# Performance work log

Hardware: AMD Instinct MI355X
Metric: run time of the kernel (lower is better)

## Reference

```python
import jax, jax.numpy as jnp
import numpy as np

H, NH, HD = 1024, 16, 64
WIN = 256
W = WIN // 2  # one-sided window
EXP = 4
PAD_VAL = 0.0  # pad_token_id
B, S0 = 2, 2048
NEG = float(np.finfo(np.float32).min)


def setup_inputs() -> dict:
    key = jax.random.key(0)
    ks = jax.random.split(key, 12)

    def lin(k, fi, fo):
        k1, k2 = jax.random.split(k)
        w = jax.random.normal(k1, (fi, fo), jnp.float32) / np.float32(np.sqrt(fi))
        b = jax.random.normal(k2, (fo,), jnp.float32) * 0.02
        return w, b

    x = jax.random.normal(ks[0], (B, S0, H), jnp.float32)
    mask = jnp.zeros((B, S0), jnp.int32)  # 0 = real token, 1 = pad
    wq, bq = lin(ks[1], H, H)
    wk, bk = lin(ks[2], H, H)
    wv, bv = lin(ks[3], H, H)
    wqg, bqg = lin(ks[4], H, H)
    wkg, bkg = lin(ks[5], H, H)
    wvg, bvg = lin(ks[6], H, H)
    ln_g = jnp.ones((H,), jnp.float32)
    ln_b = jnp.zeros((H,), jnp.float32)
    w1, b1 = lin(ks[7], H, H * EXP)
    w2, b2 = lin(ks[8], H * EXP, H)
    return dict(x=x, mask=mask, wq=wq, bq=bq, wk=wk, bk=bk, wv=wv, bv=bv,
                wqg=wqg, bqg=bqg, wkg=wkg, bkg=bkg, wvg=wvg, bvg=bvg,
                ln_g=ln_g, ln_b=ln_b, w1=w1, b1=b1, w2=w2, b2=b2)


def _forward(x, mask, wq, bq, wk, bk, wv, bv, wqg, bqg, wkg, bkg, wvg, bvg,
             ln_g, ln_b, w1, b1, w2, b2):
    Bsz, s0, _ = x.shape
    pad = WIN - s0 % WIN
    xp = jnp.pad(x, ((0, 0), (0, pad), (0, 0)), constant_values=PAD_VAL)
    m = jnp.pad(mask, ((0, 0), (0, pad)), constant_values=1)
    S = s0 + pad
    lm = (m * -10000).at[:, -1].set(10000)  # [B,S]; task='cls': last token global
    is_masked = lm < 0
    remove = lm != 0  # masked OR global keys removed from local windows

    inv_sqrt = np.float32(1.0 / np.sqrt(HD))
    q = ((xp @ wq + bq) * inv_sqrt).reshape(Bsz, S, NH, HD)
    k = (xp @ wk + bk).reshape(Bsz, S, NH, HD)
    v = (xp @ wv + bv).reshape(Bsz, S, NH, HD)

    nc = S // W
    # chunked banded scores: query chunk of W attends to 3W keys (prev/self/next)
    qc = q.transpose(0, 2, 1, 3).reshape(Bsz, NH, nc, W, HD)
    kpad = jnp.pad(k.transpose(0, 2, 1, 3), ((0, 0), (0, 0), (W, W), (0, 0)))
    idx3w = jnp.arange(nc)[:, None] * W + jnp.arange(3 * W)[None, :]  # [nc,3W]
    kc = kpad[:, :, idx3w]  # [B,NH,nc,3W,HD]
    sc = jnp.einsum('bhcpd,bhckd->bhcpk', qc, kc)  # [B,NH,nc,W,3W]
    p_idx = jnp.arange(W)[:, None]
    d_idx = jnp.arange(2 * W + 1)[None, :]
    band = sc[:, :, :, p_idx, p_idx + d_idx]  # [B,NH,nc,W,2W+1]
    band = band.reshape(Bsz, NH, S, 2 * W + 1).transpose(0, 2, 1, 3)  # [B,S,NH,2W+1]

    # key index j = i + d - W for offset d in [0, 2W]
    j = jnp.arange(S)[:, None] + jnp.arange(2 * W + 1)[None, :] - W
    in_range = (j >= 0) & (j < S)
    jc = jnp.clip(j, 0, S - 1)
    fmask = jnp.where(remove, NEG, 0.0)  # [B,S]
    band = band + fmask[:, jc][:, :, None, :]
    band = jnp.where(in_range[None, :, None, :], band, -jnp.inf)

    # global key column (single global token = last position), concatenated in front
    gcol = jnp.einsum('bshd,bhd->bsh', q, k[:, -1])[..., None]  # [B,S,NH,1]
    scores = jnp.concatenate([gcol, band], axis=-1)  # [B,S,NH,2W+2]
    probs = jax.nn.softmax(scores, axis=-1)
    probs = jnp.where(is_masked[:, :, None, None], 0.0, probs)

    out_g = probs[..., 0][..., None] * v[:, -1][:, None]  # [B,S,NH,HD]
    lp = probs[..., 1:].transpose(0, 2, 1, 3).reshape(Bsz, NH, nc, W, 2 * W + 1)
    pc = jnp.zeros((Bsz, NH, nc, W, 3 * W), probs.dtype).at[:, :, :, p_idx, p_idx + d_idx].set(lp)
    vpad = jnp.pad(v.transpose(0, 2, 1, 3), ((0, 0), (0, 0), (W, W), (0, 0)))
    vc = vpad[:, :, idx3w]  # [B,NH,nc,3W,HD]
    out_l = jnp.einsum('bhcpk,bhckd->bhcpd', pc, vc).reshape(Bsz, NH, S, HD).transpose(0, 2, 1, 3)
    attn = (out_l + out_g).reshape(Bsz, S, H)

    # full global attention for the global token (separate projections)
    qg = ((xp[:, -1] @ wqg + bqg) * inv_sqrt).reshape(Bsz, NH, HD)
    kg = (xp @ wkg + bkg).reshape(Bsz, S, NH, HD)
    vg = (xp @ wvg + bvg).reshape(Bsz, S, NH, HD)
    gs = jnp.einsum('bhd,bshd->bhs', qg, kg)
    gs = jnp.where(is_masked[:, None, :], NEG, gs)
    gout = jnp.einsum('bhs,bshd->bhd', jax.nn.softmax(gs, axis=-1), vg).reshape(Bsz, H)
    attn = attn.at[:, -1].set(gout)

    y = (xp + attn)[:, :s0]  # residual then strip padding
    mu = y.mean(-1, keepdims=True)
    var = ((y - mu) ** 2).mean(-1, keepdims=True)
    y = (y - mu) * jax.lax.rsqrt(var + 1e-5) * ln_g + ln_b
    h = jax.nn.gelu(y @ w1 + b1, approximate=False)
    return y + (h @ w2 + b2)


def reference(x, mask, wq, bq, wk, bk, wv, bv, wqg, bqg, wkg, bkg, wvg, bvg,
              ln_g, ln_b, w1, b1, w2, b2):
    return _forward(x, mask, wq, bq, wk, bk, wv, bv, wqg, bqg, wkg, bkg,
                    wvg, bvg, ln_g, ln_b, w1, b1, w2, b2)
```

## Files before the change

kernel.cpp:

```cpp
#include <hip/hip_runtime.h>


using bf16x8 = __attribute__((ext_vector_type(8))) short;
using bf16x4 = __attribute__((ext_vector_type(4))) short;
using f32x4  = __attribute__((ext_vector_type(4))) float;

__device__ __forceinline__ float b2f(short s) {
    return __uint_as_float(((unsigned int)(unsigned short)s) << 16);
}
__device__ __forceinline__ short f2b(float f) {
    unsigned int u = __float_as_uint(f);
    u += 0x7fffu + ((u >> 16) & 1u);
    return (short)(u >> 16);
}
__device__ __forceinline__ f32x4 mfma16(bf16x8 a, bf16x8 b, f32x4 c) {
    return __builtin_amdgcn_mfma_f32_16x16x32_bf16(a, b, c, 0, 0, 0);
}
__device__ __forceinline__ float safe_exp(float x) {
    return __expf((x <= 0.f) ? x : 0.f);
}
__device__ __forceinline__ float fast_gelu(float v) {
    float z  = fabsf(v) * 0.70710678118f;
    float t  = __builtin_amdgcn_rcpf(fmaf(0.47047f, z, 1.f));
    float e  = __expf(-z * z);
    float p  = t * fmaf(t, fmaf(t, 0.7478556f, -0.0958798f), 0.3480242f);
    float er = fmaf(-p, e, 1.f);
    er = (v < 0.f) ? -er : er;
    return 0.5f * v * (1.f + er);
}
__device__ __forceinline__ void load_lds16(const short* g, short* l) {
    __builtin_amdgcn_global_load_lds((const __attribute__((address_space(1))) void*)g,
                                     (__attribute__((address_space(3))) void*)l, 16, 0, 0);
}
__device__ __forceinline__ void barrier_lds_only() {
    asm volatile("s_waitcnt lgkmcnt(0)" ::: "memory");
    __builtin_amdgcn_s_barrier();
    asm volatile("" ::: "memory");
}
#define NEGF (-3.0e38f)

__global__ void cvt_f32_bf16(const float* __restrict__ in, short* __restrict__ out, int n) {
    int i = (blockIdx.x * 256 + threadIdx.x) * 4;
    f32x4 v = *(const f32x4*)(in + i);
    bf16x4 o;
#pragma unroll
    for (int j = 0; j < 4; ++j) o[j] = f2b(v[j]);
    *(bf16x4*)(out + i) = o;
}

__global__ void cvt_transpose(const float* __restrict__ in, short* __restrict__ out,
                              int R, int C) {
    __shared__ short tile[32][33];
    int bx = blockIdx.x * 32, by = blockIdx.y * 32;
    int tx = threadIdx.x, ty = threadIdx.y;
    for (int i = ty; i < 32; i += 8)
        tile[i][tx] = f2b(in[(size_t)(by + i) * C + bx + tx]);
    __syncthreads();
    for (int i = ty; i < 32; i += 8)
        out[(size_t)(bx + i) * R + by + tx] = tile[tx][i];
}

__global__ void cvt_transpose_qkv(const float* __restrict__ wq, const float* __restrict__ wk,
                                  const float* __restrict__ wv, short* __restrict__ out) {
    __shared__ short tile[32][33];
    const float* in = (blockIdx.z == 0) ? wq : (blockIdx.z == 1) ? wk : wv;
    short* dst = out + (size_t)blockIdx.z * 1024 * 1024;
    int bx = blockIdx.x * 32, by = blockIdx.y * 32;
    int tx = threadIdx.x, ty = threadIdx.y;
    for (int i = ty; i < 32; i += 8)
        tile[i][tx] = f2b(in[(size_t)(by + i) * 1024 + bx + tx]);
    __syncthreads();
    for (int i = ty; i < 32; i += 8)
        dst[(size_t)(bx + i) * 1024 + by + tx] = tile[tx][i];
}

__global__ __launch_bounds__(256, 4) void gemm_bt(
    const short* __restrict__ A, const short* __restrict__ Bt,
    const float* __restrict__ bias0, const float* __restrict__ bias1,
    const float* __restrict__ bias2,
    short* __restrict__ C, short* __restrict__ Vt,
    int M, int N, int K, float scale, int mode)
{
    __shared__ short sh[128 * 136];
    short* As = sh;
    short* Bs = sh + 8192;
    int m0 = blockIdx.x * 128, n0 = blockIdx.y * 128;
    int t = threadIdx.x;
    int wave = t >> 6, lane = t & 63, quad = lane >> 4, l16 = lane & 15;
    int wr = (wave >> 1) * 64, wc = (wave & 1) * 64;

    const short* ap[4]; const short* bp[4]; short* la[4]; short* lb[4];
    int gk = (((lane & 7) ^ (lane >> 3)) * 8);
#pragma unroll
    for (int l = 0; l < 4; ++l) {
        int c = wave * 4 + l;
        int row = c * 8 + (lane >> 3);
        ap[l] = A  + (size_t)(m0 + row) * K + gk;
        bp[l] = Bt + (size_t)(n0 + row) * K + gk;
        la[l] = As + c * 512;
        lb[l] = Bs + c * 512;
    }
    int sw = l16 & 7;

    f32x4 acc[4][4] = {};
    for (int k0 = 0; k0 < K; k0 += 64) {
#pragma unroll
        for (int l = 0; l < 4; ++l) { load_lds16(ap[l] + k0, la[l]); load_lds16(bp[l] + k0, lb[l]); }
        __syncthreads();
#pragma unroll
        for (int ks = 0; ks < 2; ++ks) {
            int slot = ((ks * 4 + quad) ^ sw) * 8;
            bf16x8 af[4], bfr[4];
#pragma unroll
            for (int i = 0; i < 4; ++i)
                af[i] = *(bf16x8*)(As + (wr + i * 16 + l16) * 64 + slot);
#pragma unroll
            for (int j = 0; j < 4; ++j)
                bfr[j] = *(bf16x8*)(Bs + (wc + j * 16 + l16) * 64 + slot);
#pragma unroll
            for (int i = 0; i < 4; ++i)
#pragma unroll
                for (int j = 0; j < 4; ++j)
                    acc[i][j] = mfma16(af[i], bfr[j], acc[i][j]);
        }
        __syncthreads();
    }

    int seg0 = n0 >> 10;
    if (mode == 1 || seg0 < 2) {
        if (mode == 1) {
#pragma unroll
            for (int j = 0; j < 4; ++j) {
                int col = n0 + wc + j * 16 + l16;
                float bs = bias0[col];
#pragma unroll
                for (int i = 0; i < 4; ++i)
#pragma unroll
                    for (int r = 0; r < 4; ++r) {
                        float v = fast_gelu(acc[i][j][r] + bs);
                        sh[(wr + i * 16 + quad * 4 + r) * 136 + wc + j * 16 + l16] = f2b(v);
                    }
            }
        } else {
            float sc = (seg0 == 0) ? scale : 1.0f;
            const float* bpt = (seg0 == 0) ? bias0 : bias1;
#pragma unroll
            for (int j = 0; j < 4; ++j) {
                int col = n0 + wc + j * 16 + l16;
                float bs = bpt[col & 1023];
#pragma unroll
                for (int i = 0; i < 4; ++i)
#pragma unroll
                    for (int r = 0; r < 4; ++r)
                        sh[(wr + i * 16 + quad * 4 + r) * 136 + wc + j * 16 + l16] =
                            f2b((acc[i][j][r] + bs) * sc);
            }
        }
        __syncthreads();
        int row = t >> 1, half = t & 1;
        const short* src = sh + row * 136 + half * 64;
        short* dst = C + (size_t)(m0 + row) * N + n0 + half * 64;
#pragma unroll
        for (int cgk = 0; cgk < 8; ++cgk)
            *(bf16x8*)(dst + cgk * 8) = *(const bf16x8*)(src + cgk * 8);
    } else {
#pragma unroll
        for (int j = 0; j < 4; ++j) {
            int cl = wc + j * 16 + l16;
            float bs = bias2[(n0 & 1023) + cl];
#pragma unroll
            for (int i = 0; i < 4; ++i)
#pragma unroll
                for (int r = 0; r < 4; ++r)
                    sh[cl * 136 + wr + i * 16 + quad * 4 + r] = f2b(acc[i][j][r] + bs);
        }
        __syncthreads();
        int h0 = (n0 & 1023) >> 6;
        int bb = m0 >> 11, s0 = m0 & 2047;
        int sc = t & 15;
#pragma unroll
        for (int cgk = 0; cgk < 8; ++cgk) {
            int cl = (t >> 4) + cgk * 16;
            int h = h0 + (cl >> 6), d = cl & 63;
            *(bf16x8*)(Vt + (((size_t)(bb * 16 + h)) * 64 + d) * 2048 + s0 + sc * 8) =
                *(const bf16x8*)(sh + cl * 136 + sc * 8);
        }
    }
}

__global__ __launch_bounds__(256, 4) void gemm64_db(
    const short* __restrict__ A, const short* __restrict__ Bt,
    const float* __restrict__ bias, const float* __restrict__ resf,
    float* __restrict__ Cf, int M, int N, int K)
{
    __shared__ short As[2][64 * 64];
    __shared__ short Bs[2][64 * 64];
    int m0 = blockIdx.x * 64, n0 = blockIdx.y * 64;
    int t = threadIdx.x;
    int wave = t >> 6, lane = t & 63, quad = lane >> 4, l16 = lane & 15;
    int wr = (wave >> 1) * 32, wc = (wave & 1) * 32;

    const short* ap[2]; const short* bp[2]; int lo[2];
    int gk = (((lane & 7) ^ (lane >> 3)) * 8);
#pragma unroll
    for (int l = 0; l < 2; ++l) {
        int c = wave * 2 + l;
        int row = c * 8 + (lane >> 3);
        ap[l] = A  + (size_t)(m0 + row) * K + gk;
        bp[l] = Bt + (size_t)(n0 + row) * K + gk;
        lo[l] = c * 512;
    }
    int sw = l16 & 7;

    const int nt = K >> 6;
#pragma unroll
    for (int l = 0; l < 2; ++l) { load_lds16(ap[l], &As[0][lo[l]]); load_lds16(bp[l], &Bs[0][lo[l]]); }

    f32x4 acc[2][2] = {};
    for (int ti = 0; ti < nt; ++ti) {
        int cur = ti & 1;
        if (ti + 1 < nt) {
            int k0 = (ti + 1) << 6;
#pragma unroll
            for (int l = 0; l < 2; ++l) {
                load_lds16(ap[l] + k0, &As[cur ^ 1][lo[l]]);
                load_lds16(bp[l] + k0, &Bs[cur ^ 1][lo[l]]);
            }
            asm volatile("s_waitcnt vmcnt(4)" ::: "memory");
        } else {
            asm volatile("s_waitcnt vmcnt(0)" ::: "memory");
        }
        __builtin_amdgcn_s_barrier();
        asm volatile("" ::: "memory");

        const short* as = &As[cur][0];
        const short* bs = &Bs[cur][0];
#pragma unroll
        for (int ks = 0; ks < 2; ++ks) {
            int slot = ((ks * 4 + quad) ^ sw) * 8;
            bf16x8 af[2], bfr[2];
#pragma unroll
            for (int i = 0; i < 2; ++i)
                af[i] = *(bf16x8*)(as + (wr + i * 16 + l16) * 64 + slot);
#pragma unroll
            for (int j = 0; j < 2; ++j)
                bfr[j] = *(bf16x8*)(bs + (wc + j * 16 + l16) * 64 + slot);
#pragma unroll
            for (int i = 0; i < 2; ++i)
#pragma unroll
                for (int j = 0; j < 2; ++j)
                    acc[i][j] = mfma16(af[i], bfr[j], acc[i][j]);
        }
        asm volatile("" ::: "memory");
        __builtin_amdgcn_s_barrier();
    }

#pragma unroll
    for (int j = 0; j < 2; ++j) {
        int col = n0 + wc + j * 16 + l16;
        float bs = bias[col];
#pragma unroll
        for (int i = 0; i < 2; ++i) {
#pragma unroll
            for (int r = 0; r < 4; ++r) {
                int row = m0 + wr + i * 16 + quad * 4 + r;
                Cf[(size_t)row * N + col] = acc[i][j][r] + bs + resf[(size_t)row * N + col];
            }
        }
    }
}

__global__ __launch_bounds__(256, 4) void attn_kernel(
    const short* __restrict__ QKV, const short* __restrict__ Vt,
    const int* __restrict__ mask,
    const float* __restrict__ bk, const float* __restrict__ bv,
    short* __restrict__ attn)
{
    extern __shared__ char smem[];
    short* PsQ = (short*)smem;
    short* KV  = (short*)(smem + 17408);
    float* gkf = (float*)(smem + 35840);
    float* gvf = (float*)(smem + 36096);

    int blk = blockIdx.x;
    int c = blk & 31, h = (blk >> 5) & 15, b = blk >> 9;
    int t = threadIdx.x;
    int wave = t >> 6, lane = t & 63, quad = lane >> 4, l16 = lane & 15;
    int q0 = c * 64;
    const int bs_off = b * 2048;
    const short* Q = QKV + h * 64;
    const short* K = QKV + 1024 + h * 64;
    const short* Vg = Vt + (size_t)(b * 16 + h) * 64 * 2048;

#pragma unroll
    for (int l = 0; l < 2; ++l) {
        int idx = l * 256 + t;
        int p = idx >> 3, dc = (idx & 7) * 8;
        *(bf16x8*)(PsQ + p * 72 + dc) =
            *(const bf16x8*)(Q + ((size_t)(bs_off + q0 + p)) * 3072 + dc);
    }
    if (t < 64) { gkf[t] = bk[h * 64 + t]; gvf[t] = bv[h * 64 + t]; }
    __syncthreads();

    bf16x8 aq[2];
#pragma unroll
    for (int ks = 0; ks < 2; ++ks)
        aq[ks] = *(bf16x8*)(PsQ + (wave * 16 + l16) * 72 + ks * 32 + quad * 8);

    float s_g[4];
#pragma unroll
    for (int r = 0; r < 4; ++r) {
        int row = wave * 16 + quad * 4 + r;
        float part = 0.f;
#pragma unroll
        for (int dd = 0; dd < 4; ++dd) {
            int d = l16 * 4 + dd;
            part += b2f(PsQ[row * 72 + d]) * gkf[d];
        }
#pragma unroll
        for (int dsh = 1; dsh < 16; dsh <<= 1) part += __shfl_xor(part, dsh);
        s_g[r] = part;
    }

    f32x4 o_acc[4] = {};
    float m_run[4], l_run[4];
#pragma unroll
    for (int r = 0; r < 4; ++r) { m_run[r] = NEGF; l_run[r] = 0.f; }

    int kt_beg = (q0 == 0) ? 1 : 0;
    int kt_end = (q0 + 128 < 2048) ? 3 : 2;

    bf16x8 kreg[4], vreg[4];
    {
        int jb = q0 + (kt_beg - 1) * 128;
#pragma unroll
        for (int l = 0; l < 4; ++l) {
            int idx = l * 256 + t;
            int row = jb + (idx >> 3);
            row = (row < 0) ? 0 : ((row > 2047) ? 2047 : row);
            kreg[l] = *(const bf16x8*)(K + ((size_t)(bs_off + row)) * 3072 + (idx & 7) * 8);
        }
    }

    for (int kt = kt_beg; kt < kt_end; ++kt) {
        int jb = q0 + (kt - 1) * 128;
#pragma unroll
        for (int l = 0; l < 4; ++l) {
            int idx = l * 256 + t;
            *(bf16x8*)(KV + (idx >> 3) * 72 + (idx & 7) * 8) = kreg[l];
        }
#pragma unroll
        for (int l = 0; l < 4; ++l) {
            int idx = l * 256 + t;
            int s0 = jb + (idx & 15) * 8;
            s0 = (s0 < 0) ? 0 : ((s0 > 2040) ? 2040 : s0);
            vreg[l] = *(const bf16x8*)(Vg + ((size_t)(idx >> 4)) * 2048 + s0);
        }
        barrier_lds_only();

        f32x4 s_acc[8] = {};
#pragma unroll
        for (int ks = 0; ks < 2; ++ks) {
            bf16x8 bk8[8];
#pragma unroll
            for (int tj = 0; tj < 8; ++tj)
                bk8[tj] = *(bf16x8*)(KV + (tj * 16 + l16) * 72 + ks * 32 + quad * 8);
#pragma unroll
            for (int tj = 0; tj < 8; ++tj)
                s_acc[tj] = mfma16(aq[ks], bk8[tj], s_acc[tj]);
        }

        float negj[8]; int jcol[8];
#pragma unroll
        for (int tj = 0; tj < 8; ++tj) {
            jcol[tj] = jb + tj * 16 + l16;
            bool jv = (jcol[tj] >= 0) && (jcol[tj] < 2048);
            int jc = jv ? jcol[tj] : 0;
            negj[tj] = (!jv || (mask[bs_off + jc] != 0)) ? NEGF : 0.f;
        }
        float tmax[4];
#pragma unroll
        for (int r = 0; r < 4; ++r) tmax[r] = NEGF;
        int irow_base = q0 + wave * 16 + quad * 4;
#pragma unroll
        for (int tj = 0; tj < 8; ++tj)
#pragma unroll
            for (int r = 0; r < 4; ++r) {
                int dj = jcol[tj] - (irow_base + r);
                float sc = (dj >= -128 && dj <= 128) ? (s_acc[tj][r] + negj[tj]) : NEGF;
                s_acc[tj][r] = sc;
                tmax[r] = fmaxf(tmax[r], sc);
            }
#pragma unroll
        for (int r = 0; r < 4; ++r)
#pragma unroll
            for (int dsh = 1; dsh < 16; dsh <<= 1)
                tmax[r] = fmaxf(tmax[r], __shfl_xor(tmax[r], dsh));

        float alpha[4], lsum[4];
#pragma unroll
        for (int r = 0; r < 4; ++r) {
            float mnew = fmaxf(m_run[r], tmax[r]);
            alpha[r] = safe_exp(m_run[r] - mnew);
            m_run[r] = mnew;
            lsum[r] = 0.f;
        }
#pragma unroll
        for (int tj = 0; tj < 8; ++tj)
#pragma unroll
            for (int r = 0; r < 4; ++r) {
                float p = safe_exp(s_acc[tj][r] - m_run[r]);
                lsum[r] += p;
                PsQ[(wave * 16 + quad * 4 + r) * 136 + tj * 16 + l16] = f2b(p);
            }
#pragma unroll
        for (int r = 0; r < 4; ++r) {
#pragma unroll
            for (int dsh = 1; dsh < 16; dsh <<= 1) lsum[r] += __shfl_xor(lsum[r], dsh);
            l_run[r] = l_run[r] * alpha[r] + lsum[r];
        }
#pragma unroll
        for (int dj = 0; dj < 4; ++dj)
#pragma unroll
            for (int r = 0; r < 4; ++r) o_acc[dj][r] *= alpha[r];

        barrier_lds_only();

#pragma unroll
        for (int l = 0; l < 4; ++l) {
            int idx = l * 256 + t;
            *(bf16x8*)(KV + (idx >> 4) * 136 + (idx & 15) * 8) = vreg[l];
        }
        if (kt + 1 < kt_end) {
            int jb2 = q0 + kt * 128;
#pragma unroll
            for (int l = 0; l < 4; ++l) {
                int idx = l * 256 + t;
                int row = jb2 + (idx >> 3);
                row = (row < 0) ? 0 : ((row > 2047) ? 2047 : row);
                kreg[l] = *(const bf16x8*)(K + ((size_t)(bs_off + row)) * 3072 + (idx & 7) * 8);
            }
        }
        barrier_lds_only();

#pragma unroll
        for (int ks = 0; ks < 4; ++ks) {
            bf16x8 ap, bv8[4];
            ap = *(bf16x8*)(PsQ + (wave * 16 + l16) * 136 + ks * 32 + quad * 8);
#pragma unroll
            for (int dj = 0; dj < 4; ++dj)
                bv8[dj] = *(bf16x8*)(KV + (dj * 16 + l16) * 136 + ks * 32 + quad * 8);
#pragma unroll
            for (int dj = 0; dj < 4; ++dj)
                o_acc[dj] = mfma16(ap, bv8[dj], o_acc[dj]);
        }
        barrier_lds_only();
    }

    int irow_base = q0 + wave * 16 + quad * 4;
#pragma unroll
    for (int r = 0; r < 4; ++r) {
        int i = irow_base + r;
        float m2 = fmaxf(m_run[r], s_g[r]);
        float pg = safe_exp(s_g[r] - m2);
        float al = safe_exp(m_run[r] - m2);
        float l2 = l_run[r] * al + pg;
        float invl = 1.f / fmaxf(l2, 1e-30f);
        float qm = (mask[bs_off + i] > 0) ? 0.f : 1.f;
#pragma unroll
        for (int dj = 0; dj < 4; ++dj) {
            int d = dj * 16 + l16;
            float val = (o_acc[dj][r] * al + pg * gvf[d]) * invl * qm;
            attn[((size_t)(bs_off + i)) * 1024 + h * 64 + d] = f2b(val);
        }
    }
}

__global__ __launch_bounds__(256) void resid_ln(
    const float* __restrict__ x, const short* __restrict__ attn,
    const float* __restrict__ g, const float* __restrict__ be,
    short* __restrict__ yb, float* __restrict__ yf)
{
    int row = blockIdx.x, t = threadIdx.x;
    int lane = t & 63, wave = t >> 6;
    const size_t base = (size_t)row * 1024;
    float v[4]; float s = 0.f, s2 = 0.f;
#pragma unroll
    for (int i = 0; i < 4; ++i) {
        int c = i * 256 + t;
        float val = x[base + c] + b2f(attn[base + c]);
        v[i] = val; s += val; s2 += val * val;
    }
#pragma unroll
    for (int off = 32; off > 0; off >>= 1) { s += __shfl_xor(s, off); s2 += __shfl_xor(s2, off); }
    __shared__ float red[8];
    if (lane == 0) { red[wave] = s; red[4 + wave] = s2; }
    __syncthreads();
    s  = red[0] + red[1] + red[2] + red[3];
    s2 = red[4] + red[5] + red[6] + red[7];
    float mu  = s * (1.f / 1024.f);
    float var = s2 * (1.f / 1024.f) - mu * mu;
    float inv = rsqrtf(fmaxf(var, 0.f) + 1e-5f);
#pragma unroll
    for (int i = 0; i < 4; ++i) {
        int c = i * 256 + t;
        float o = (v[i] - mu) * inv * g[c] + be[c];
        yb[base + c] = f2b(o);
        yf[base + c] = o;
    }
}

static constexpr size_t MEG      = 1048576;
static constexpr size_t OFF_WQKV = 0;
static constexpr size_t OFF_W1T  = 3 * MEG;
static constexpr size_t OFF_W2T  = 7 * MEG;
static constexpr size_t OFF_XB   = 11 * MEG;
static constexpr size_t OFF_QKV  = 15 * MEG;
static constexpr size_t OFF_VT   = 27 * MEG;
static constexpr size_t OFF_ATT  = 31 * MEG;
static constexpr size_t OFF_YN   = 35 * MEG;
static constexpr size_t OFF_YF   = 39 * MEG;
static constexpr size_t OFF_H    = OFF_QKV;

extern "C" void kernel_launch(void* const* d_in, const int* in_sizes, int n_in,
                              void* d_out, int out_size, void* d_ws, size_t ws_size,
                              hipStream_t stream) {
    (void)in_sizes; (void)n_in; (void)out_size; (void)ws_size;
    const float* x    = (const float*)d_in[0];
    const int*   mask = (const int*)  d_in[1];
    const float* wq   = (const float*)d_in[2];
    const float* bq   = (const float*)d_in[3];
    const float* wk   = (const float*)d_in[4];
    const float* bk   = (const float*)d_in[5];
    const float* wv   = (const float*)d_in[6];
    const float* bv   = (const float*)d_in[7];
    const float* lng  = (const float*)d_in[14];
    const float* lnb  = (const float*)d_in[15];
    const float* w1   = (const float*)d_in[16];
    const float* b1   = (const float*)d_in[17];
    const float* w2   = (const float*)d_in[18];
    const float* b2   = (const float*)d_in[19];
    short* ws  = (short*)d_ws;
    float* out = (float*)d_out;

    dim3 tb(32, 8);
    cvt_transpose_qkv<<<dim3(32, 32, 3), tb, 0, stream>>>(wq, wk, wv, ws + OFF_WQKV);
    cvt_transpose<<<dim3(128, 32), tb, 0, stream>>>(w1, ws + OFF_W1T, 1024, 4096);
    cvt_transpose<<<dim3(32, 128), tb, 0, stream>>>(w2, ws + OFF_W2T, 4096, 1024);
    cvt_f32_bf16<<<4096, 256, 0, stream>>>(x, ws + OFF_XB, 4194304);

    gemm_bt<<<dim3(32, 24), 256, 0, stream>>>(ws + OFF_XB, ws + OFF_WQKV,
                                              bq, bk, bv,
                                              ws + OFF_QKV, ws + OFF_VT,
                                              4096, 3072, 1024, 0.125f, 0);

    attn_kernel<<<1024, 256, 36352, stream>>>(ws + OFF_QKV, ws + OFF_VT,
                                              mask, bk, bv, ws + OFF_ATT);

    resid_ln<<<4096, 256, 0, stream>>>(x, ws + OFF_ATT, lng, lnb,
                                       ws + OFF_YN, (float*)(ws + OFF_YF));

    gemm_bt<<<dim3(32, 32), 256, 0, stream>>>(ws + OFF_YN, ws + OFF_W1T,
                                              b1, nullptr, nullptr,
                                              ws + OFF_H, nullptr,
                                              4096, 4096, 1024, 1.0f, 1);
    gemm64_db<<<dim3(64, 16), 256, 0, stream>>>(ws + OFF_H, ws + OFF_W2T,
                                                b2, (const float*)(ws + OFF_YF),
                                                out, 4096, 1024, 4096);
}
```

Measured before the change: 345.9 us.

## Stream K/V tiles directly to LDS with async loads and XOR swizzle

The attention kernel now loads K and V tiles straight from global memory into separate swizzled LDS buffers through direct-to-LDS loads, instead of staging them in registers and writing them to a shared KV buffer. vmcnt waits and raw barriers overlap the next K tile with the PV matmul and the next V tile with the following QK step. The XOR swizzle replaces row padding to avoid bank conflicts. LDS use grows to about 50KB per block and launch bounds drop to 3 blocks per CU, which may reduce occupancy. It relies on load_lds16 being defined elsewhere in the file.

```diff
diff --git a/kernel.cpp b/kernel.cpp
--- a/kernel.cpp
+++ b/kernel.cpp
@@ -270,7 +270,7 @@
     }
 }
 
-__global__ __launch_bounds__(256, 4) void attn_kernel(
+__global__ __launch_bounds__(256, 3) void attn_kernel(
     const short* __restrict__ QKV, const short* __restrict__ Vt,
     const int* __restrict__ mask,
     const float* __restrict__ bk, const float* __restrict__ bv,
@@ -278,9 +278,10 @@
 {
     extern __shared__ char smem[];
     short* PsQ = (short*)smem;
-    short* KV  = (short*)(smem + 17408);
-    float* gkf = (float*)(smem + 35840);
-    float* gvf = (float*)(smem + 36096);
+    short* Ks  = (short*)(smem + 17408);
+    short* Vs  = (short*)(smem + 33792);
+    float* gkf = (float*)(smem + 50176);
+    float* gvf = (float*)(smem + 50432);
 
     int blk = blockIdx.x;
     int c = blk & 31, h = (blk >> 5) & 15, b = blk >> 9;
@@ -291,6 +292,8 @@
     const short* Q = QKV + h * 64;
     const short* K = QKV + 1024 + h * 64;
     const short* Vg = Vt + (size_t)(b * 16 + h) * 64 * 2048;
+    int sw = l16 & 7;
+    int wub = (t & 192) * 8;
 
 #pragma unroll
     for (int l = 0; l < 2; ++l) {
@@ -330,41 +333,50 @@
     int kt_beg = (q0 == 0) ? 1 : 0;
     int kt_end = (q0 + 128 < 2048) ? 3 : 2;
 
-    bf16x8 kreg[4], vreg[4];
+#define ISSUE_K(JB)                                                          \
+    {                                                                        \
+        _Pragma("unroll")                                                    \
+        for (int l = 0; l < 4; ++l) {                                        \
+            int row = l * 32 + (t >> 3);                                     \
+            int rg = (JB) + row;                                             \
+            rg = (rg < 0) ? 0 : ((rg > 2047) ? 2047 : rg);                   \
+            load_lds16(K + (size_t)(bs_off + rg) * 3072 +                    \
+                           (((t & 7) ^ (row & 7)) * 8),                      \
+                       Ks + l * 2048 + wub);                                 \
+        }                                                                    \
+    }
+#define ISSUE_V(JB)                                                          \
+    {                                                                        \
+        _Pragma("unroll")                                                    \
+        for (int l = 0; l < 4; ++l) {                                        \
+            int d = l * 16 + (t >> 4);                                       \
+            int sg = (JB) + (((t & 15) ^ (d & 7)) * 8);                      \
+            sg = (sg < 0) ? 0 : ((sg > 2040) ? 2040 : sg);                   \
+            load_lds16(Vg + (size_t)d * 2048 + sg,                           \
+                       Vs + l * 2048 + wub);                                 \
+        }                                                                    \
+    }
+
     {
-        int jb = q0 + (kt_beg - 1) * 128;
-#pragma unroll
-        for (int l = 0; l < 4; ++l) {
-            int idx = l * 256 + t;
-            int row = jb + (idx >> 3);
-            row = (row < 0) ? 0 : ((row > 2047) ? 2047 : row);
-            kreg[l] = *(const bf16x8*)(K + ((size_t)(bs_off + row)) * 3072 + (idx & 7) * 8);
-        }
+        int jb0 = q0 + (kt_beg - 1) * 128;
+        ISSUE_K(jb0);
+        ISSUE_V(jb0);
     }
 
     for (int kt = kt_beg; kt < kt_end; ++kt) {
         int jb = q0 + (kt - 1) * 128;
-#pragma unroll
-        for (int l = 0; l < 4; ++l) {
-            int idx = l * 256 + t;
-            *(bf16x8*)(KV + (idx >> 3) * 72 + (idx & 7) * 8) = kreg[l];
-        }
-#pragma unroll
-        for (int l = 0; l < 4; ++l) {
-            int idx = l * 256 + t;
-            int s0 = jb + (idx & 15) * 8;
-            s0 = (s0 < 0) ? 0 : ((s0 > 2040) ? 2040 : s0);
-            vreg[l] = *(const bf16x8*)(Vg + ((size_t)(idx >> 4)) * 2048 + s0);
-        }
-        barrier_lds_only();
+        asm volatile("s_waitcnt vmcnt(4)" ::: "memory");
+        __builtin_amdgcn_s_barrier();
+        asm volatile("" ::: "memory");
 
         f32x4 s_acc[8] = {};
 #pragma unroll
         for (int ks = 0; ks < 2; ++ks) {
+            int slot = ((ks * 4 + quad) ^ sw) * 8;
             bf16x8 bk8[8];
 #pragma unroll
             for (int tj = 0; tj < 8; ++tj)
-                bk8[tj] = *(bf16x8*)(KV + (tj * 16 + l16) * 72 + ks * 32 + quad * 8);
+                bk8[tj] = *(bf16x8*)(Ks + (tj * 16 + l16) * 64 + slot);
 #pragma unroll
             for (int tj = 0; tj < 8; ++tj)
                 s_acc[tj] = mfma16(aq[ks], bk8[tj], s_acc[tj]);
@@ -426,35 +438,30 @@
 
         barrier_lds_only();
 
-#pragma unroll
-        for (int l = 0; l < 4; ++l) {
-            int idx = l * 256 + t;
-            *(bf16x8*)(KV + (idx >> 4) * 136 + (idx & 15) * 8) = vreg[l];
-        }
         if (kt + 1 < kt_end) {
-            int jb2 = q0 + kt * 128;
-#pragma unroll
-            for (int l = 0; l < 4; ++l) {
-                int idx = l * 256 + t;
-                int row = jb2 + (idx >> 3);
-                row = (row < 0) ? 0 : ((row > 2047) ? 2047 : row);
-                kreg[l] = *(const bf16x8*)(K + ((size_t)(bs_off + row)) * 3072 + (idx & 7) * 8);
-            }
-        }
-        barrier_lds_only();
+            ISSUE_K(jb + 128);
+            asm volatile("s_waitcnt vmcnt(4)" ::: "memory");
+        } else {
+            asm volatile("s_waitcnt vmcnt(0)" ::: "memory");
+        }
+        __builtin_amdgcn_s_barrier();
+        asm volatile("" ::: "memory");
 
 #pragma unroll
         for (int ks = 0; ks < 4; ++ks) {
-            bf16x8 ap, bv8[4];
-            ap = *(bf16x8*)(PsQ + (wave * 16 + l16) * 136 + ks * 32 + quad * 8);
+            int slot = ((ks * 4 + quad) ^ sw) * 8;
+            bf16x8 ap = *(bf16x8*)(PsQ + (wave * 16 + l16) * 136 + ks * 32 + quad * 8);
+            bf16x8 bv8[4];
 #pragma unroll
             for (int dj = 0; dj < 4; ++dj)
-                bv8[dj] = *(bf16x8*)(KV + (dj * 16 + l16) * 136 + ks * 32 + quad * 8);
+                bv8[dj] = *(bf16x8*)(Vs + (dj * 16 + l16) * 128 + slot);
 #pragma unroll
             for (int dj = 0; dj < 4; ++dj)
                 o_acc[dj] = mfma16(ap, bv8[dj], o_acc[dj]);
         }
         barrier_lds_only();
+
+        if (kt + 1 < kt_end) ISSUE_V(jb + 128);
     }
 
     int irow_base = q0 + wave * 16 + quad * 4;
@@ -474,6 +481,8 @@
             attn[((size_t)(bs_off + i)) * 1024 + h * 64 + d] = f2b(val);
         }
     }
+#undef ISSUE_K
+#undef ISSUE_V
 }
 
 __global__ __launch_bounds__(256) void resid_ln(
@@ -554,7 +563,7 @@
                                               ws + OFF_QKV, ws + OFF_VT,
                                               4096, 3072, 1024, 0.125f, 0);
 
-    attn_kernel<<<1024, 256, 36352, stream>>>(ws + OFF_QKV, ws + OFF_VT,
+    attn_kernel<<<1024, 256, 50688, stream>>>(ws + OFF_QKV, ws + OFF_VT,
                                               mask, bk, bv, ws + OFF_ATT);
 
     resid_ln<<<4096, 256, 0, stream>>>(x, ws + OFF_ATT, lng, lnb,
```

Result: faster. 330.1 us (-4.6%).
